# Kernel optimization log

Hardware: AMD Instinct MI355X
Metric: run time of the kernel (lower is better)

## Reference

```python
import jax, jax.numpy as jnp
import numpy as np

N_HEADS = 16
THETA = 10000.0


def _rope(x, cos, sin):
    # x: [B,H,S,hd]; pairs are interleaved (x[...,2i], x[...,2i+1]) = complex pair
    xe = x[..., 0::2]
    xo = x[..., 1::2]
    re = xe * cos - xo * sin
    im = xe * sin + xo * cos
    return jnp.stack([re, im], axis=-1).reshape(x.shape)


def setup_inputs() -> dict:
    key = jax.random.key(0)
    k1, k2, k3 = jax.random.split(key, 3)
    B, S, D = 2, 2048, 2048
    x = jax.random.normal(k1, (B, S, D), dtype=jnp.float32)
    Wqkv = jax.random.normal(k2, (D, 3 * D), dtype=jnp.float32) * (D ** -0.5)
    Wo = jax.random.normal(k3, (D, D), dtype=jnp.float32) * (D ** -0.5)
    return {"x": x, "Wqkv": Wqkv, "Wo": Wo}


def reference(x, Wqkv, Wo):
    B, S, D = x.shape
    H = N_HEADS
    hd = D // H
    half = hd // 2

    qkv = x @ Wqkv                                   # [B,S,3D]
    q, k, v = jnp.split(qkv, 3, axis=-1)
    # [B,S,D] -> [B,H,S,hd]
    q = q.reshape(B, S, H, hd).transpose(0, 2, 1, 3)
    k = k.reshape(B, S, H, hd).transpose(0, 2, 1, 3)
    v = v.reshape(B, S, H, hd).transpose(0, 2, 1, 3)

    # RoPE frequencies: thetas = theta^(-2i/hd), freqs = pos outer thetas
    i = jnp.arange(half, dtype=jnp.float32)
    inv = THETA ** (-2.0 * i / hd)
    pos = jnp.arange(S, dtype=jnp.float32)
    freqs = pos[:, None] * inv[None, :]              # [S, half]
    cos = jnp.cos(freqs)[None, None]                 # [1,1,S,half]
    sin = jnp.sin(freqs)[None, None]
    q = _rope(q, cos, sin)
    k = _rope(k, cos, sin)

    scale = 1.0 / jnp.sqrt(jnp.float32(hd))
    scores = jnp.einsum("bhqd,bhkd->bhqk", q, k) * scale
    causal = jnp.tril(jnp.ones((S, S), dtype=bool))
    scores = jnp.where(causal[None, None], scores, -jnp.inf)
    attn = jax.nn.softmax(scores, axis=-1)
    y = jnp.einsum("bhqk,bhkd->bhqd", attn, v)       # [B,H,S,hd]
    y = y.transpose(0, 2, 1, 3).reshape(B, S, D)
    return y @ Wo
```

## Files before the change

### kernel.cpp

```cpp
#include <hip/hip_runtime.h>
#include <hip/hip_bf16.h>

typedef __attribute__((ext_vector_type(4))) float f32x4;
typedef __attribute__((ext_vector_type(8))) short s16x8;
typedef unsigned short u16;
typedef unsigned int u32;

#define MFMA16 __builtin_amdgcn_mfma_f32_16x16x32_bf16

#define GLL16(g, l)                                                        \
  __builtin_amdgcn_global_load_lds(                                        \
      (const __attribute__((address_space(1))) void*)(g),                  \
      (__attribute__((address_space(3))) void*)(l), 16, 0, 0)

__device__ __forceinline__ u16 f2b(float f) {
  u32 x = __builtin_bit_cast(u32, f);
  u32 r = (x + 0x7fffu + ((x >> 16) & 1u)) >> 16;
  return (u16)r;
}
__device__ __forceinline__ float b2f(u16 u) {
  u32 x = ((u32)u) << 16;
  return __builtin_bit_cast(float, x);
}

__global__ __launch_bounds__(256) void k_cvt(const float* __restrict__ in, u16* __restrict__ out) {
  size_t i = ((size_t)blockIdx.x * 256 + threadIdx.x) * 4;
  float4 v = *(const float4*)(in + i);
  ushort4 o; o.x = f2b(v.x); o.y = f2b(v.y); o.z = f2b(v.z); o.w = f2b(v.w);
  *(ushort4*)(out + i) = o;
}

__global__ __launch_bounds__(256) void k_tconv(const float* __restrict__ in, u16* __restrict__ out,
                                               int R, int C) {
  __shared__ u16 tile[64][72];
  int c0 = blockIdx.x * 64, r0 = blockIdx.y * 64;
  int t = threadIdx.x;
#pragma unroll
  for (int p = 0; p < 4; ++p) {
    int idx = p * 1024 + t * 4;
    int row = idx >> 6, col = idx & 63;
    float4 v = *(const float4*)&in[(size_t)(r0 + row) * C + c0 + col];
    tile[row][col]     = f2b(v.x);
    tile[row][col + 1] = f2b(v.y);
    tile[row][col + 2] = f2b(v.z);
    tile[row][col + 3] = f2b(v.w);
  }
  __syncthreads();
#pragma unroll
  for (int p = 0; p < 4; ++p) {
    int idx = p * 1024 + t * 4;
    int row = idx >> 6, col = idx & 63;
    ushort4 o;
    o.x = tile[col][row]; o.y = tile[col + 1][row];
    o.z = tile[col + 2][row]; o.w = tile[col + 3][row];
    *(ushort4*)&out[(size_t)(c0 + row) * R + r0 + col] = o;
  }
}

__global__ __launch_bounds__(256) void k_trv(const u16* __restrict__ v, u16* __restrict__ vt) {
  __shared__ u16 tile[64][72];
  int bh = blockIdx.z;
  int s0 = blockIdx.x * 64, d0 = blockIdx.y * 64;
  const u16* src = v + (size_t)bh * 2048 * 128;
  u16* dst = vt + (size_t)bh * 2048 * 128;
  int t = threadIdx.x;
#pragma unroll
  for (int p = 0; p < 4; ++p) {
    int idx = p * 1024 + t * 4;
    int row = idx >> 6, col = idx & 63;
    ushort4 x = *(const ushort4*)&src[(size_t)(s0 + row) * 128 + d0 + col];
    tile[row][col] = x.x; tile[row][col + 1] = x.y;
    tile[row][col + 2] = x.z; tile[row][col + 3] = x.w;
  }
  __syncthreads();
#pragma unroll
  for (int p = 0; p < 4; ++p) {
    int idx = p * 1024 + t * 4;
    int row = idx >> 6, col = idx & 63;
    ushort4 o;
    o.x = tile[col][row]; o.y = tile[col + 1][row];
    o.z = tile[col + 2][row]; o.w = tile[col + 3][row];
    *(ushort4*)&dst[(size_t)(d0 + row) * 2048 + s0 + col] = o;
  }
}

__global__ __launch_bounds__(256) void k_trig(float2* __restrict__ tab) {
  int t = blockIdx.x * 256 + threadIdx.x;
  int s = t >> 6, i = t & 63;
  float inv = expf(-(float)i * (9.210340371976184f / 64.f));
  float a = (float)s * inv;
  float sn, cs;
  sincosf(a, &sn, &cs);
  tab[t] = make_float2(cs, sn);
}

__global__ __launch_bounds__(256) void k_rope(u16* __restrict__ q, u16* __restrict__ k,
                                              const float2* __restrict__ tab) {
  u16* ptr = blockIdx.y ? k : q;
  size_t tid = (size_t)blockIdx.x * 256 + threadIdx.x;
  int g = (int)(tid & 15);
  int s = (int)((tid >> 4) & 2047);
  int bh = (int)(tid >> 15);
  size_t base = ((size_t)bh * 2048 + s) * 128 + (size_t)g * 8;
  uint4 dv = *(const uint4*)(ptr + base);
  u16* pu = (u16*)&dv;
  const float2* tb = &tab[s * 64 + g * 4];
#pragma unroll
  for (int j = 0; j < 4; ++j) {
    float xe = b2f(pu[2 * j]), xo = b2f(pu[2 * j + 1]);
    float c = tb[j].x, sn = tb[j].y;
    pu[2 * j]     = f2b(xe * c - xo * sn);
    pu[2 * j + 1] = f2b(xe * sn + xo * c);
  }
  *(uint4*)(ptr + base) = dv;
}

template <int MODE>
__global__ __launch_bounds__(256) void k_gemm97b(const u16* __restrict__ A, const u16* __restrict__ Bt,
                                                 u16* __restrict__ qo, u16* __restrict__ ko,
                                                 u16* __restrict__ vo, float* __restrict__ C) {
  constexpr int K = 2048;
  __shared__ u16 sa[128 * 64];
  __shared__ u16 sb[128 * 64];
  int tid = threadIdx.x;
  int lane = tid & 63, w = tid >> 6;
  int wm = (w >> 1) * 64, wn = (w & 1) * 64;
  int lr = lane & 15, lg = lane >> 4;
  int n0 = blockIdx.x * 128;
  int m0 = blockIdx.y * 128;

  int srow = tid >> 3;
  int swzb = ((tid & 7) << 4) ^ ((srow & 7) << 4);
  const char* gA = (const char*)(A + (size_t)(m0 + srow) * K) + swzb;
  const char* gB = (const char*)(Bt + (size_t)(n0 + srow) * K) + swzb;

  int colb0 = (lg << 4) ^ ((lr & 7) << 4);
  int aRowB = (wm + lr) * 128;
  int bRowB = (wn + lr) * 128;

  f32x4 acc[4][4] = {};
  for (int k0 = 0; k0 < K; k0 += 64) {
    __syncthreads();
#pragma unroll
    for (int r = 0; r < 4; ++r) {
      GLL16(gA + ((size_t)(r * 32) * K + k0) * 2, (char*)sa + r * 4096 + tid * 16);
      GLL16(gB + ((size_t)(r * 32) * K + k0) * 2, (char*)sb + r * 4096 + tid * 16);
    }
    __syncthreads();
#pragma unroll
    for (int ks = 0; ks < 2; ++ks) {
      int cb = colb0 ^ (ks << 6);
      s16x8 af[4], bf[4];
#pragma unroll
      for (int i = 0; i < 4; ++i) af[i] = *(const s16x8*)((const char*)sa + aRowB + i * 2048 + cb);
#pragma unroll
      for (int i = 0; i < 4; ++i) bf[i] = *(const s16x8*)((const char*)sb + bRowB + i * 2048 + cb);
#pragma unroll
      for (int mi = 0; mi < 4; ++mi)
#pragma unroll
        for (int ni = 0; ni < 4; ++ni)
          acc[mi][ni] = MFMA16(af[mi], bf[ni], acc[mi][ni], 0, 0, 0);
    }
  }

  if constexpr (MODE == 0) {
    int which = blockIdx.x >> 4;
    int h = blockIdx.x & 15;
    u16* dst = which == 0 ? qo : (which == 1 ? ko : vo);
#pragma unroll
    for (int mi = 0; mi < 4; ++mi)
#pragma unroll
      for (int ni = 0; ni < 4; ++ni)
#pragma unroll
        for (int r = 0; r < 4; ++r) {
          int m = m0 + wm + mi * 16 + lg * 4 + r;
          int d = wn + ni * 16 + lr;
          int b = m >> 11, s = m & 2047;
          dst[(((size_t)b * 16 + h) * 2048 + s) * 128 + d] = f2b(acc[mi][ni][r]);
        }
  } else {
#pragma unroll
    for (int mi = 0; mi < 4; ++mi)
#pragma unroll
      for (int ni = 0; ni < 4; ++ni)
#pragma unroll
        for (int r = 0; r < 4; ++r) {
          int m = m0 + wm + mi * 16 + lg * 4 + r;
          int n = n0 + wn + ni * 16 + lr;
          C[(size_t)m * 2048 + n] = acc[mi][ni][r];
        }
  }
}

__global__ __launch_bounds__(256) void k_attn(const u16* __restrict__ q, const u16* __restrict__ k,
                                              const u16* __restrict__ vt, u16* __restrict__ y) {
  constexpr int S = 2048, HD = 128;
  __shared__ u16 kt[2][64][128];
  __shared__ u16 vtl[2][128][64];
  __shared__ u16 pl[4][16][72];
  int bh = blockIdx.x;
  int qt = (gridDim.y - 1) - blockIdx.y;
  int q0 = qt * 64;
  int t = threadIdx.x, lane = t & 63, w = t >> 6;
  int lr = lane & 15, lg = lane >> 4;
  const size_t base = (size_t)bh * S * HD;
  const u16* kbh = k + base;
  const u16* vbh = vt + base;

  int kr_l = ((w * 4) << 2) + (lane >> 4);
  int kcb_base = (lane & 15) << 4;
  int vr_l = ((w * 4) << 3) + (lane >> 3);
  int vcb_base = (lane & 7) << 4;

  s16x8 aq[4];
  {
    size_t qrow = base + (size_t)(q0 + w * 16 + lr) * HD;
#pragma unroll
    for (int i = 0; i < 4; ++i) aq[i] = *(const s16x8*)&q[qrow + i * 32 + lg * 8];
  }
  f32x4 o[8] = {};
  float mrow[4] = {-INFINITY, -INFINITY, -INFINITY, -INFINITY};
  float lsum[4] = {};
  const float scale = 0.08838834764831845f;
  int kv_end = q0 + 64;

#define STAGE_KV(buf, kv)                                                             \
  {                                                                                   \
    _Pragma("unroll")                                                                 \
    for (int i = 0; i < 4; ++i) {                                                     \
      int kr = kr_l + 4 * i;                                                          \
      int kcb = kcb_base ^ ((kr & 7) << 4);                                           \
      GLL16((const char*)(kbh + (size_t)((kv) + kr) * HD) + kcb,                      \
            (char*)&kt[buf][0][0] + ((w * 4 + i) << 10) + (lane << 4));               \
      int vr = vr_l + 8 * i;                                                          \
      int vcb = vcb_base ^ ((vr & 7) << 4);                                           \
      GLL16((const char*)(vbh + (size_t)vr * S + (kv)) + vcb,                         \
            (char*)&vtl[buf][0][0] + ((w * 4 + i) << 10) + (lane << 4));              \
    }                                                                                 \
  }

  STAGE_KV(0, 0);
  int cur = 0;
  for (int kv0 = 0; kv0 < kv_end; kv0 += 64) {
    __syncthreads();
    if (kv0 + 64 < kv_end) STAGE_KV(cur ^ 1, kv0 + 64);
    f32x4 sf[4] = {};
    int swz = (lr & 7) << 4;
    __builtin_amdgcn_s_setprio(1);
#pragma unroll
    for (int dstep = 0; dstep < 4; ++dstep)
#pragma unroll
      for (int nt = 0; nt < 4; ++nt) {
        int cb = ((dstep << 6) + (lg << 4)) ^ swz;
        s16x8 bk = *(const s16x8*)((const char*)&kt[cur][nt * 16 + lr][0] + cb);
        sf[nt] = MFMA16(aq[dstep], bk, sf[nt], 0, 0, 0);
      }
    __builtin_amdgcn_s_setprio(0);
    int grow0 = q0 + w * 16 + lg * 4;
    float pmax[4] = {-INFINITY, -INFINITY, -INFINITY, -INFINITY};
#pragma unroll
    for (int nt = 0; nt < 4; ++nt) {
      int col = kv0 + nt * 16 + lr;
#pragma unroll
      for (int r = 0; r < 4; ++r) {
        float sv = sf[nt][r] * scale;
        if (col > grow0 + r) sv = -INFINITY;
        sf[nt][r] = sv;
        pmax[r] = fmaxf(pmax[r], sv);
      }
    }
#pragma unroll
    for (int off = 1; off < 16; off <<= 1)
#pragma unroll
      for (int r = 0; r < 4; ++r) pmax[r] = fmaxf(pmax[r], __shfl_xor(pmax[r], off));
    float alpha[4], ps[4];
#pragma unroll
    for (int r = 0; r < 4; ++r) {
      float mn = fmaxf(mrow[r], pmax[r]);
      alpha[r] = __expf(mrow[r] - mn);
      mrow[r] = mn;
      ps[r] = 0.f;
#pragma unroll
      for (int nt = 0; nt < 4; ++nt) { float e = __expf(sf[nt][r] - mn); sf[nt][r] = e; ps[r] += e; }
    }
#pragma unroll
    for (int off = 1; off < 16; off <<= 1)
#pragma unroll
      for (int r = 0; r < 4; ++r) ps[r] += __shfl_xor(ps[r], off);
#pragma unroll
    for (int r = 0; r < 4; ++r) {
      lsum[r] = lsum[r] * alpha[r] + ps[r];
#pragma unroll
      for (int dt = 0; dt < 8; ++dt) o[dt][r] *= alpha[r];
    }
#pragma unroll
    for (int nt = 0; nt < 4; ++nt)
#pragma unroll
      for (int r = 0; r < 4; ++r)
        pl[w][lg * 4 + r][nt * 16 + lr] = f2b(sf[nt][r]);
    asm volatile("s_waitcnt lgkmcnt(0)" ::: "memory");
    __builtin_amdgcn_sched_barrier(0);
    s16x8 pa0 = *(const s16x8*)&pl[w][lr][lg * 8];
    s16x8 pa1 = *(const s16x8*)&pl[w][lr][32 + lg * 8];
    __builtin_amdgcn_s_setprio(1);
#pragma unroll
    for (int dt = 0; dt < 8; ++dt) {
      int cb0 = (lg << 4) ^ swz;
      int cb1 = (64 + (lg << 4)) ^ swz;
      s16x8 bv0 = *(const s16x8*)((const char*)&vtl[cur][dt * 16 + lr][0] + cb0);
      s16x8 bv1 = *(const s16x8*)((const char*)&vtl[cur][dt * 16 + lr][0] + cb1);
      o[dt] = MFMA16(pa0, bv0, o[dt], 0, 0, 0);
      o[dt] = MFMA16(pa1, bv1, o[dt], 0, 0, 0);
    }
    __builtin_amdgcn_s_setprio(0);
    cur ^= 1;
  }
#undef STAGE_KV
  int b = bh >> 4, h = bh & 15;
#pragma unroll
  for (int dt = 0; dt < 8; ++dt)
#pragma unroll
    for (int r = 0; r < 4; ++r) {
      int srow = q0 + w * 16 + lg * 4 + r;
      float val = o[dt][r] / lsum[r];
      y[((size_t)(b * 2048 + srow)) * 2048 + h * 128 + dt * 16 + lr] = f2b(val);
    }
}

extern "C" void kernel_launch(void* const* d_in, const int* in_sizes, int n_in,
                              void* d_out, int out_size, void* d_ws, size_t ws_size,
                              hipStream_t stream) {
  const float* x    = (const float*)d_in[0];
  const float* wqkv = (const float*)d_in[1];
  const float* wo   = (const float*)d_in[2];
  float* out = (float*)d_out;
  char* ws = (char*)d_ws;
  u16* xb    = (u16*)(ws);
  u16* wqkvt = (u16*)(ws + (size_t)(16)  * 1048576);
  u16* wot   = (u16*)(ws + (size_t)(40)  * 1048576);
  u16* qb    = (u16*)(ws + (size_t)(48)  * 1048576);
  u16* kb    = (u16*)(ws + (size_t)(64)  * 1048576);
  u16* vb    = (u16*)(ws + (size_t)(80)  * 1048576);
  u16* vtb   = (u16*)(ws + (size_t)(96)  * 1048576);
  u16* yb    = (u16*)(ws + (size_t)(112) * 1048576);
  float2* trig = (float2*)(ws + (size_t)(128) * 1048576);

  k_cvt<<<8192, 256, 0, stream>>>(x, xb);
  k_tconv<<<dim3(96, 32), 256, 0, stream>>>(wqkv, wqkvt, 2048, 6144);
  k_tconv<<<dim3(32, 32), 256, 0, stream>>>(wo, wot, 2048, 2048);
  k_trig<<<512, 256, 0, stream>>>(trig);
  k_gemm97b<0><<<dim3(48, 32), 256, 0, stream>>>(xb, wqkvt, qb, kb, vb, nullptr);
  k_rope<<<dim3(4096, 2), 256, 0, stream>>>(qb, kb, trig);
  k_trv<<<dim3(32, 2, 32), 256, 0, stream>>>(vb, vtb);
  k_attn<<<dim3(32, 32), 256, 0, stream>>>(qb, kb, vtb, yb);
  k_gemm97b<1><<<dim3(16, 32), 256, 0, stream>>>(yb, wot, nullptr, nullptr, nullptr, out);
}
```

Before: 285.5 us.

## Fuse RoPE into QKV GEMM epilogue and enlarge attention blocks to 128 queries

```diff
diff --git a/kernel.cpp b/kernel.cpp
--- a/kernel.cpp
+++ b/kernel.cpp
@@ -94,31 +94,11 @@
   tab[t] = make_float2(cs, sn);
 }
 
-__global__ __launch_bounds__(256) void k_rope(u16* __restrict__ q, u16* __restrict__ k,
-                                              const float2* __restrict__ tab) {
-  u16* ptr = blockIdx.y ? k : q;
-  size_t tid = (size_t)blockIdx.x * 256 + threadIdx.x;
-  int g = (int)(tid & 15);
-  int s = (int)((tid >> 4) & 2047);
-  int bh = (int)(tid >> 15);
-  size_t base = ((size_t)bh * 2048 + s) * 128 + (size_t)g * 8;
-  uint4 dv = *(const uint4*)(ptr + base);
-  u16* pu = (u16*)&dv;
-  const float2* tb = &tab[s * 64 + g * 4];
-#pragma unroll
-  for (int j = 0; j < 4; ++j) {
-    float xe = b2f(pu[2 * j]), xo = b2f(pu[2 * j + 1]);
-    float c = tb[j].x, sn = tb[j].y;
-    pu[2 * j]     = f2b(xe * c - xo * sn);
-    pu[2 * j + 1] = f2b(xe * sn + xo * c);
-  }
-  *(uint4*)(ptr + base) = dv;
-}
-
 template <int MODE>
 __global__ __launch_bounds__(256) void k_gemm97b(const u16* __restrict__ A, const u16* __restrict__ Bt,
                                                  u16* __restrict__ qo, u16* __restrict__ ko,
-                                                 u16* __restrict__ vo, float* __restrict__ C) {
+                                                 u16* __restrict__ vo, float* __restrict__ C,
+                                                 const float2* __restrict__ trig) {
   constexpr int K = 2048;
   __shared__ u16 sa[128 * 64];
   __shared__ u16 sb[128 * 64];
@@ -167,17 +147,26 @@
     int which = blockIdx.x >> 4;
     int h = blockIdx.x & 15;
     u16* dst = which == 0 ? qo : (which == 1 ? ko : vo);
+    bool dorope = (which < 2);
+    float sgn = (lr & 1) ? 1.f : -1.f;
 #pragma unroll
     for (int mi = 0; mi < 4; ++mi)
 #pragma unroll
-      for (int ni = 0; ni < 4; ++ni)
+      for (int ni = 0; ni < 4; ++ni) {
+        int d = wn + ni * 16 + lr;
 #pragma unroll
         for (int r = 0; r < 4; ++r) {
           int m = m0 + wm + mi * 16 + lg * 4 + r;
-          int d = wn + ni * 16 + lr;
           int b = m >> 11, s = m & 2047;
-          dst[(((size_t)b * 16 + h) * 2048 + s) * 128 + d] = f2b(acc[mi][ni][r]);
-        }
+          float v = acc[mi][ni][r];
+          float other = __shfl_xor(v, 1);
+          if (dorope) {
+            float2 cs = trig[s * 64 + (d >> 1)];
+            v = v * cs.x + sgn * other * cs.y;
+          }
+          dst[(((size_t)b * 16 + h) * 2048 + s) * 128 + d] = f2b(v);
+        }
+      }
   } else {
 #pragma unroll
     for (int mi = 0; mi < 4; ++mi)
@@ -192,25 +181,39 @@
   }
 }
 
-__global__ __launch_bounds__(256) void k_attn(const u16* __restrict__ q, const u16* __restrict__ k,
+__global__ __launch_bounds__(512) void k_attn(const u16* __restrict__ q, const u16* __restrict__ k,
                                               const u16* __restrict__ vt, u16* __restrict__ y) {
   constexpr int S = 2048, HD = 128;
   __shared__ u16 kt[2][64][128];
   __shared__ u16 vtl[2][128][64];
-  __shared__ u16 pl[4][16][72];
+  __shared__ u16 pl[8][16][64];
   int bh = blockIdx.x;
   int qt = (gridDim.y - 1) - blockIdx.y;
-  int q0 = qt * 64;
+  int q0 = qt * 128;
   int t = threadIdx.x, lane = t & 63, w = t >> 6;
   int lr = lane & 15, lg = lane >> 4;
   const size_t base = (size_t)bh * S * HD;
   const u16* kbh = k + base;
   const u16* vbh = vt + base;
-
-  int kr_l = ((w * 4) << 2) + (lane >> 4);
-  int kcb_base = (lane & 15) << 4;
-  int vr_l = ((w * 4) << 3) + (lane >> 3);
-  int vcb_base = (lane & 7) << 4;
+  char* plb = (char*)&pl[0][0][0] + w * 2048;
+
+  int krow_l = t >> 4;
+  int kcolb = (t & 15) << 4;
+  int vrow_l = t >> 3;
+  int vcolb = (t & 7) << 4;
+
+#define STAGE_KV(buf, kv)                                                              \
+  {                                                                                    \
+    _Pragma("unroll")                                                                  \
+    for (int i = 0; i < 2; ++i) {                                                      \
+      int kr = krow_l + i * 32;                                                        \
+      GLL16((const char*)(kbh + (size_t)((kv) + kr) * HD) + (kcolb ^ ((kr & 7) << 4)), \
+            (char*)&kt[buf][0][0] + i * 8192 + t * 16);                                \
+      int vr = vrow_l + i * 64;                                                        \
+      GLL16((const char*)(vbh + (size_t)vr * S + (kv)) + (vcolb ^ ((vr & 7) << 4)),    \
+            (char*)&vtl[buf][0][0] + i * 8192 + t * 16);                               \
+    }                                                                                  \
+  }
 
   s16x8 aq[4];
   {
@@ -222,97 +225,89 @@
   float mrow[4] = {-INFINITY, -INFINITY, -INFINITY, -INFINITY};
   float lsum[4] = {};
   const float scale = 0.08838834764831845f;
-  int kv_end = q0 + 64;
-
-#define STAGE_KV(buf, kv)                                                             \
-  {                                                                                   \
-    _Pragma("unroll")                                                                 \
-    for (int i = 0; i < 4; ++i) {                                                     \
-      int kr = kr_l + 4 * i;                                                          \
-      int kcb = kcb_base ^ ((kr & 7) << 4);                                           \
-      GLL16((const char*)(kbh + (size_t)((kv) + kr) * HD) + kcb,                      \
-            (char*)&kt[buf][0][0] + ((w * 4 + i) << 10) + (lane << 4));               \
-      int vr = vr_l + 8 * i;                                                          \
-      int vcb = vcb_base ^ ((vr & 7) << 4);                                           \
-      GLL16((const char*)(vbh + (size_t)vr * S + (kv)) + vcb,                         \
-            (char*)&vtl[buf][0][0] + ((w * 4 + i) << 10) + (lane << 4));              \
-    }                                                                                 \
-  }
+  int kv_end = q0 + 128;
+  int qw_hi = q0 + w * 16 + 15;
 
   STAGE_KV(0, 0);
   int cur = 0;
   for (int kv0 = 0; kv0 < kv_end; kv0 += 64) {
     __syncthreads();
     if (kv0 + 64 < kv_end) STAGE_KV(cur ^ 1, kv0 + 64);
-    f32x4 sf[4] = {};
-    int swz = (lr & 7) << 4;
-    __builtin_amdgcn_s_setprio(1);
-#pragma unroll
-    for (int dstep = 0; dstep < 4; ++dstep)
+    if (kv0 <= qw_hi) {
+      f32x4 sf[4] = {};
+      int swz = (lr & 7) << 4;
+      __builtin_amdgcn_s_setprio(1);
+#pragma unroll
+      for (int dstep = 0; dstep < 4; ++dstep)
+#pragma unroll
+        for (int nt = 0; nt < 4; ++nt) {
+          int cb = ((dstep << 6) + (lg << 4)) ^ swz;
+          s16x8 bk = *(const s16x8*)((const char*)&kt[cur][nt * 16 + lr][0] + cb);
+          sf[nt] = MFMA16(aq[dstep], bk, sf[nt], 0, 0, 0);
+        }
+      __builtin_amdgcn_s_setprio(0);
+      int grow0 = q0 + w * 16 + lg * 4;
+      float pmax[4] = {-INFINITY, -INFINITY, -INFINITY, -INFINITY};
 #pragma unroll
       for (int nt = 0; nt < 4; ++nt) {
-        int cb = ((dstep << 6) + (lg << 4)) ^ swz;
-        s16x8 bk = *(const s16x8*)((const char*)&kt[cur][nt * 16 + lr][0] + cb);
-        sf[nt] = MFMA16(aq[dstep], bk, sf[nt], 0, 0, 0);
-      }
-    __builtin_amdgcn_s_setprio(0);
-    int grow0 = q0 + w * 16 + lg * 4;
-    float pmax[4] = {-INFINITY, -INFINITY, -INFINITY, -INFINITY};
-#pragma unroll
-    for (int nt = 0; nt < 4; ++nt) {
-      int col = kv0 + nt * 16 + lr;
+        int col = kv0 + nt * 16 + lr;
+#pragma unroll
+        for (int r = 0; r < 4; ++r) {
+          float sv = sf[nt][r] * scale;
+          if (col > grow0 + r) sv = -INFINITY;
+          sf[nt][r] = sv;
+          pmax[r] = fmaxf(pmax[r], sv);
+        }
+      }
+#pragma unroll
+      for (int off = 1; off < 16; off <<= 1)
+#pragma unroll
+        for (int r = 0; r < 4; ++r) pmax[r] = fmaxf(pmax[r], __shfl_xor(pmax[r], off));
+      float alpha[4], ps[4];
 #pragma unroll
       for (int r = 0; r < 4; ++r) {
-        float sv = sf[nt][r] * scale;
-        if (col > grow0 + r) sv = -INFINITY;
-        sf[nt][r] = sv;
-        pmax[r] = fmaxf(pmax[r], sv);
-      }
+        float mn = fmaxf(mrow[r], pmax[r]);
+        alpha[r] = __expf(mrow[r] - mn);
+        mrow[r] = mn;
+        ps[r] = 0.f;
+#pragma unroll
+        for (int nt = 0; nt < 4; ++nt) { float e = __expf(sf[nt][r] - mn); sf[nt][r] = e; ps[r] += e; }
+      }
+#pragma unroll
+      for (int off = 1; off < 16; off <<= 1)
+#pragma unroll
+        for (int r = 0; r < 4; ++r) ps[r] += __shfl_xor(ps[r], off);
+#pragma unroll
+      for (int r = 0; r < 4; ++r) {
+        lsum[r] = lsum[r] * alpha[r] + ps[r];
+#pragma unroll
+        for (int dt = 0; dt < 8; ++dt) o[dt][r] *= alpha[r];
+      }
+#pragma unroll
+      for (int nt = 0; nt < 4; ++nt)
+#pragma unroll
+        for (int r = 0; r < 4; ++r) {
+          int row = lg * 4 + r;
+          int cb2 = ((nt * 16 + lr) * 2) ^ ((row & 7) << 4);
+          *(u16*)(plb + row * 128 + cb2) = f2b(sf[nt][r]);
+        }
+      asm volatile("s_waitcnt lgkmcnt(0)" ::: "memory");
+      __builtin_amdgcn_sched_barrier(0);
+      int pswz = (lr & 7) << 4;
+      s16x8 pa0 = *(const s16x8*)(plb + lr * 128 + ((lg * 16) ^ pswz));
+      s16x8 pa1 = *(const s16x8*)(plb + lr * 128 + ((64 + lg * 16) ^ pswz));
+      __builtin_amdgcn_s_setprio(1);
+#pragma unroll
+      for (int dt = 0; dt < 8; ++dt) {
+        int cb0 = (lg << 4) ^ swz;
+        int cb1 = (64 + (lg << 4)) ^ swz;
+        s16x8 bv0 = *(const s16x8*)((const char*)&vtl[cur][dt * 16 + lr][0] + cb0);
+        s16x8 bv1 = *(const s16x8*)((const char*)&vtl[cur][dt * 16 + lr][0] + cb1);
+        o[dt] = MFMA16(pa0, bv0, o[dt], 0, 0, 0);
+        o[dt] = MFMA16(pa1, bv1, o[dt], 0, 0, 0);
+      }
+      __builtin_amdgcn_s_setprio(0);
     }
-#pragma unroll
-    for (int off = 1; off < 16; off <<= 1)
-#pragma unroll
-      for (int r = 0; r < 4; ++r) pmax[r] = fmaxf(pmax[r], __shfl_xor(pmax[r], off));
-    float alpha[4], ps[4];
-#pragma unroll
-    for (int r = 0; r < 4; ++r) {
-      float mn = fmaxf(mrow[r], pmax[r]);
-      alpha[r] = __expf(mrow[r] - mn);
-      mrow[r] = mn;
-      ps[r] = 0.f;
-#pragma unroll
-      for (int nt = 0; nt < 4; ++nt) { float e = __expf(sf[nt][r] - mn); sf[nt][r] = e; ps[r] += e; }
-    }
-#pragma unroll
-    for (int off = 1; off < 16; off <<= 1)
-#pragma unroll
-      for (int r = 0; r < 4; ++r) ps[r] += __shfl_xor(ps[r], off);
-#pragma unroll
-    for (int r = 0; r < 4; ++r) {
-      lsum[r] = lsum[r] * alpha[r] + ps[r];
-#pragma unroll
-      for (int dt = 0; dt < 8; ++dt) o[dt][r] *= alpha[r];
-    }
-#pragma unroll
-    for (int nt = 0; nt < 4; ++nt)
-#pragma unroll
-      for (int r = 0; r < 4; ++r)
-        pl[w][lg * 4 + r][nt * 16 + lr] = f2b(sf[nt][r]);
-    asm volatile("s_waitcnt lgkmcnt(0)" ::: "memory");
-    __builtin_amdgcn_sched_barrier(0);
-    s16x8 pa0 = *(const s16x8*)&pl[w][lr][lg * 8];
-    s16x8 pa1 = *(const s16x8*)&pl[w][lr][32 + lg * 8];
-    __builtin_amdgcn_s_setprio(1);
-#pragma unroll
-    for (int dt = 0; dt < 8; ++dt) {
-      int cb0 = (lg << 4) ^ swz;
-      int cb1 = (64 + (lg << 4)) ^ swz;
-      s16x8 bv0 = *(const s16x8*)((const char*)&vtl[cur][dt * 16 + lr][0] + cb0);
-      s16x8 bv1 = *(const s16x8*)((const char*)&vtl[cur][dt * 16 + lr][0] + cb1);
-      o[dt] = MFMA16(pa0, bv0, o[dt], 0, 0, 0);
-      o[dt] = MFMA16(pa1, bv1, o[dt], 0, 0, 0);
-    }
-    __builtin_amdgcn_s_setprio(0);
     cur ^= 1;
   }
 #undef STAGE_KV
@@ -345,13 +340,12 @@
   u16* yb    = (u16*)(ws + (size_t)(112) * 1048576);
   float2* trig = (float2*)(ws + (size_t)(128) * 1048576);
 
+  k_trig<<<512, 256, 0, stream>>>(trig);
   k_cvt<<<8192, 256, 0, stream>>>(x, xb);
   k_tconv<<<dim3(96, 32), 256, 0, stream>>>(wqkv, wqkvt, 2048, 6144);
   k_tconv<<<dim3(32, 32), 256, 0, stream>>>(wo, wot, 2048, 2048);
-  k_trig<<<512, 256, 0, stream>>>(trig);
-  k_gemm97b<0><<<dim3(48, 32), 256, 0, stream>>>(xb, wqkvt, qb, kb, vb, nullptr);
-  k_rope<<<dim3(4096, 2), 256, 0, stream>>>(qb, kb, trig);
+  k_gemm97b<0><<<dim3(48, 32), 256, 0, stream>>>(xb, wqkvt, qb, kb, vb, nullptr, trig);
   k_trv<<<dim3(32, 2, 32), 256, 0, stream>>>(vb, vtb);
-  k_attn<<<dim3(32, 32), 256, 0, stream>>>(qb, kb, vtb, yb);
-  k_gemm97b<1><<<dim3(16, 32), 256, 0, stream>>>(yb, wot, nullptr, nullptr, nullptr, out);
-}
+  k_attn<<<dim3(32, 16), 512, 0, stream>>>(qb, kb, vtb, yb);
+  k_gemm97b<1><<<dim3(16, 32), 256, 0, stream>>>(yb, wot, nullptr, nullptr, nullptr, out, nullptr);
+}
```

Result: slower. 332.2 us (+16.4%).
